# Performance work log

Measured on AMD Instinct MI355X. Metric: run time of the kernel, lower is better.

The kernel has to match this reference:

```python
import jax, jax.numpy as jnp
import numpy as np

N, C, H, K = 65432, 64, 4, 256
D = C // H
POS_BND = 20            # int((4*256)**(1/3) * 2)
RPE_NUM = 2 * POS_BND + 1


def setup_inputs() -> dict:
    key = jax.random.key(0)
    ks = jax.random.split(key, 8)
    feat = jax.random.normal(ks[0], (N, C), jnp.float32)
    qkv_w = jax.random.normal(ks[1], (3 * C, C), jnp.float32) * (C ** -0.5)
    qkv_b = jnp.zeros((3 * C,), jnp.float32)
    proj_w = jax.random.normal(ks[2], (C, C), jnp.float32) * (C ** -0.5)
    proj_b = jnp.zeros((C,), jnp.float32)
    rpe_table = jax.random.normal(ks[3], (3 * RPE_NUM, H), jnp.float32) * 0.02
    order = jax.random.permutation(ks[4], N).astype(jnp.int32)
    inverse = jnp.argsort(order).astype(jnp.int32)
    grid_coord = jax.random.randint(ks[5], (N, 3), 0, 64, jnp.int32)
    batch = jnp.sort(jax.random.randint(ks[6], (N,), 0, 4, jnp.int32))
    return {
        "feat": feat, "qkv_w": qkv_w, "qkv_b": qkv_b,
        "proj_w": proj_w, "proj_b": proj_b, "rpe_table": rpe_table,
        "order": order, "inverse": inverse,
        "grid_coord": grid_coord, "batch": batch, "num_batches": 4,
    }


def reference(feat, qkv_w, qkv_b, proj_w, proj_b, rpe_table,
              order, inverse, grid_coord, batch, num_batches):
    scale = D ** -0.5
    pad = K - N % K                      # torch pads K - N%K rows
    Npad = N + pad
    P = Npad // K                        # number of serialized patches

    # gather by serialization order, pad, window
    f = jnp.concatenate([feat[order], jnp.zeros((pad, C), feat.dtype)], 0)
    f = f.reshape(P, K, C)

    # attn mask from batch ids (pad rows get id = num_batches -> masked)
    b = jnp.concatenate([batch, jnp.full((pad,), num_batches, batch.dtype)], 0)
    b = b.reshape(P, K)
    mask = jnp.where(b[:, :, None] != b[:, None, :], -1000.0, 0.0)  # [P,K,K]

    # relative positions within each window
    gc = jnp.concatenate([grid_coord[order],
                          jnp.zeros((pad, 3), grid_coord.dtype)], 0)
    gc = gc.reshape(P, K, 3)
    rel = gc[:, :, None, :] - gc[:, None, :, :]          # [P,K,K,3]
    idx = jnp.clip(rel, -POS_BND, POS_BND) + POS_BND     # [P,K,K,3]

    # RPE bias: sum of 3 per-axis table lookups (avoids [P,K,K,3,H] blowup)
    bias = rpe_table[idx[..., 0]]
    bias = bias + rpe_table[idx[..., 1] + RPE_NUM]
    bias = bias + rpe_table[idx[..., 2] + 2 * RPE_NUM]   # [P,K,K,H]
    bias = bias.transpose(0, 3, 1, 2)                    # [P,H,K,K]

    # qkv projection and head split
    qkv = (f @ qkv_w.T + qkv_b).reshape(P, K, 3, H, D)
    qkv = qkv.transpose(2, 0, 3, 1, 4)                   # [3,P,H,K,D]
    q, k, v = qkv[0], qkv[1], qkv[2]

    attn = jnp.einsum('phid,phjd->phij', q * scale, k)
    attn = attn + bias + mask[:, None]
    attn = jax.nn.softmax(attn, axis=-1)

    out = jnp.einsum('phij,phjd->phid', attn, v)         # [P,H,K,D]
    out = out.transpose(0, 2, 1, 3).reshape(Npad, C)
    out = out[inverse][:N]                               # unserialize
    return out @ proj_w.T + proj_b
```

## Files before the change

kernel.cpp:

```cpp
#include <hip/hip_runtime.h>
#include <hip/hip_bf16.h>

#define N_PTS   65432
#define C_DIM   64
#define H_HEADS 4
#define D_HEAD  16
#define K_WIN   256
#define NPAD    65536
#define P_PATCH 256
#define POS_BND 20
#define RPE_NUM 41
#define QKV_DIM 192

__global__ __launch_bounds__(256) void qkv_kernel(
    const float* __restrict__ feat, const float* __restrict__ qkv_w,
    const float* __restrict__ qkv_b, const int* __restrict__ order,
    float* __restrict__ qkv)
{
    __shared__ float fS[64 * 68];
    __shared__ float wS[192 * 68];
    __shared__ float bS[192];

    const int t  = threadIdx.x;
    const int bx = blockIdx.x;

    #pragma unroll
    for (int s = 0; s < 48; ++s) {
        int idx = t + 256 * s;
        int row = idx >> 6, col = idx & 63;
        wS[row * 68 + col] = qkv_w[idx];
    }
    if (t < QKV_DIM) bS[t] = qkv_b[t];

    {
        int rr = t >> 2, part = t & 3;
        int r = bx * 64 + rr;
        int orig = (r < N_PTS) ? order[r] : -1;
        float4 v0, v1, v2, v3;
        if (orig >= 0) {
            const float4* fp = (const float4*)(feat + (size_t)orig * 64 + part * 16);
            v0 = fp[0]; v1 = fp[1]; v2 = fp[2]; v3 = fp[3];
        } else {
            v0 = make_float4(0.f, 0.f, 0.f, 0.f); v1 = v0; v2 = v0; v3 = v0;
        }
        float* dst = fS + rr * 68 + part * 16;
        *(float4*)(dst + 0) = v0; *(float4*)(dst + 4)  = v1;
        *(float4*)(dst + 8) = v2; *(float4*)(dst + 12) = v3;
    }
    __syncthreads();

    const int rg = t >> 4, cg = t & 15;
    float acc[4][12];
    #pragma unroll
    for (int i = 0; i < 4; ++i)
        #pragma unroll
        for (int j = 0; j < 12; ++j) acc[i][j] = 0.f;

    #pragma unroll
    for (int kk = 0; kk < 16; ++kk) {
        float4 f4[4];
        #pragma unroll
        for (int i = 0; i < 4; ++i)
            f4[i] = *(const float4*)&fS[(rg * 4 + i) * 68 + kk * 4];
        #pragma unroll
        for (int j = 0; j < 12; ++j) {
            float4 w4 = *(const float4*)&wS[(cg + 16 * j) * 68 + kk * 4];
            #pragma unroll
            for (int i = 0; i < 4; ++i) {
                acc[i][j] = fmaf(f4[i].x, w4.x, acc[i][j]);
                acc[i][j] = fmaf(f4[i].y, w4.y, acc[i][j]);
                acc[i][j] = fmaf(f4[i].z, w4.z, acc[i][j]);
                acc[i][j] = fmaf(f4[i].w, w4.w, acc[i][j]);
            }
        }
    }
    #pragma unroll
    for (int i = 0; i < 4; ++i) {
        int r = bx * 64 + rg * 4 + i;
        #pragma unroll
        for (int j = 0; j < 12; ++j) {
            int c = cg + 16 * j;
            qkv[(size_t)r * QKV_DIM + c] = acc[i][j] + bS[c];
        }
    }
}

__global__ __launch_bounds__(128) void attn_kernel(
    const float* __restrict__ qkv, const float* __restrict__ rpe_table,
    const int* __restrict__ order, const int* __restrict__ grid_coord,
    const int* __restrict__ batch, float* __restrict__ attn_out)
{
    __shared__ float kS[256 * 16];
    __shared__ float vS[256 * 16];
    __shared__ int4  gS[256];
    __shared__ float rpeS[3 * RPE_NUM];

    const int t = threadIdx.x;
    const int p = blockIdx.x, h = blockIdx.y;

    for (int rr = t; rr < 256; rr += 128) {
        int r = p * 256 + rr;
        const float* row = qkv + (size_t)r * QKV_DIM;
        #pragma unroll
        for (int d4 = 0; d4 < 4; ++d4) {
            *(float4*)&kS[rr * 16 + d4 * 4] = *(const float4*)(row + 64  + h * 16 + d4 * 4);
            *(float4*)&vS[rr * 16 + d4 * 4] = *(const float4*)(row + 128 + h * 16 + d4 * 4);
        }
        if (r < N_PTS) {
            int orig = order[r];
            gS[rr] = make_int4(grid_coord[orig * 3 + 0], grid_coord[orig * 3 + 1],
                               grid_coord[orig * 3 + 2], batch[r]);
        } else {
            gS[rr] = make_int4(0, 0, 0, -1);
        }
    }
    for (int i = t; i < 3 * RPE_NUM; i += 128) rpeS[i] = rpe_table[i * H_HEADS + h];
    __syncthreads();

    const float scale = 0.25f;
    const int r0 = p * 256 + t, r1 = r0 + 128;
    const bool ok0 = r0 < N_PTS, ok1 = r1 < N_PTS;

    float q0[16], q1[16];
    {
        const float* a = qkv + (size_t)r0 * QKV_DIM + h * 16;
        const float* b = qkv + (size_t)r1 * QKV_DIM + h * 16;
        #pragma unroll
        for (int d4 = 0; d4 < 4; ++d4) {
            float4 qa = *(const float4*)(a + d4 * 4);
            float4 qb = *(const float4*)(b + d4 * 4);
            q0[d4*4+0] = qa.x * scale; q0[d4*4+1] = qa.y * scale;
            q0[d4*4+2] = qa.z * scale; q0[d4*4+3] = qa.w * scale;
            q1[d4*4+0] = qb.x * scale; q1[d4*4+1] = qb.y * scale;
            q1[d4*4+2] = qb.z * scale; q1[d4*4+3] = qb.w * scale;
        }
    }
    const int4 g0 = gS[t], g1 = gS[t + 128];

    float m0 = -1e30f, l0 = 0.f, m1 = -1e30f, l1 = 0.f;
    float acc0[16], acc1[16];
    #pragma unroll
    for (int d = 0; d < 16; ++d) { acc0[d] = 0.f; acc1[d] = 0.f; }

    for (int j = 0; j < 256; ++j) {
        const int4 gj = gS[j];

        int dx0 = min(max(g0.x - gj.x, -POS_BND), POS_BND);
        int dy0 = min(max(g0.y - gj.y, -POS_BND), POS_BND);
        int dz0 = min(max(g0.z - gj.z, -POS_BND), POS_BND);
        float s0 = rpeS[dx0 + POS_BND] + rpeS[dy0 + POS_BND + RPE_NUM]
                 + rpeS[dz0 + POS_BND + 2 * RPE_NUM];
        s0 += (g0.w == gj.w) ? 0.f : -1000.f;

        int dx1 = min(max(g1.x - gj.x, -POS_BND), POS_BND);
        int dy1 = min(max(g1.y - gj.y, -POS_BND), POS_BND);
        int dz1 = min(max(g1.z - gj.z, -POS_BND), POS_BND);
        float s1 = rpeS[dx1 + POS_BND] + rpeS[dy1 + POS_BND + RPE_NUM]
                 + rpeS[dz1 + POS_BND + 2 * RPE_NUM];
        s1 += (g1.w == gj.w) ? 0.f : -1000.f;

        const float4* kp = (const float4*)&kS[j * 16];
        float4 k0 = kp[0], k1v = kp[1], k2 = kp[2], k3 = kp[3];
        s0 = fmaf(q0[0],  k0.x,  s0); s0 = fmaf(q0[1],  k0.y,  s0);
        s0 = fmaf(q0[2],  k0.z,  s0); s0 = fmaf(q0[3],  k0.w,  s0);
        s0 = fmaf(q0[4],  k1v.x, s0); s0 = fmaf(q0[5],  k1v.y, s0);
        s0 = fmaf(q0[6],  k1v.z, s0); s0 = fmaf(q0[7],  k1v.w, s0);
        s0 = fmaf(q0[8],  k2.x,  s0); s0 = fmaf(q0[9],  k2.y,  s0);
        s0 = fmaf(q0[10], k2.z,  s0); s0 = fmaf(q0[11], k2.w,  s0);
        s0 = fmaf(q0[12], k3.x,  s0); s0 = fmaf(q0[13], k3.y,  s0);
        s0 = fmaf(q0[14], k3.z,  s0); s0 = fmaf(q0[15], k3.w,  s0);
        s1 = fmaf(q1[0],  k0.x,  s1); s1 = fmaf(q1[1],  k0.y,  s1);
        s1 = fmaf(q1[2],  k0.z,  s1); s1 = fmaf(q1[3],  k0.w,  s1);
        s1 = fmaf(q1[4],  k1v.x, s1); s1 = fmaf(q1[5],  k1v.y, s1);
        s1 = fmaf(q1[6],  k1v.z, s1); s1 = fmaf(q1[7],  k1v.w, s1);
        s1 = fmaf(q1[8],  k2.x,  s1); s1 = fmaf(q1[9],  k2.y,  s1);
        s1 = fmaf(q1[10], k2.z,  s1); s1 = fmaf(q1[11], k2.w,  s1);
        s1 = fmaf(q1[12], k3.x,  s1); s1 = fmaf(q1[13], k3.y,  s1);
        s1 = fmaf(q1[14], k3.z,  s1); s1 = fmaf(q1[15], k3.w,  s1);

        bool nd = (s0 > m0) || (s1 > m1);
        if (__any(nd)) {
            float mn0 = fmaxf(m0, s0);
            float c0  = __expf(m0 - mn0);
            l0 *= c0;
            #pragma unroll
            for (int d = 0; d < 16; ++d) acc0[d] *= c0;
            m0 = mn0;
            float mn1 = fmaxf(m1, s1);
            float c1  = __expf(m1 - mn1);
            l1 *= c1;
            #pragma unroll
            for (int d = 0; d < 16; ++d) acc1[d] *= c1;
            m1 = mn1;
        }
        float p0 = __expf(s0 - m0); l0 += p0;
        float p1 = __expf(s1 - m1); l1 += p1;

        const float4* vp = (const float4*)&vS[j * 16];
        float4 va = vp[0], vb = vp[1], vc = vp[2], vd = vp[3];
        acc0[0]  = fmaf(p0, va.x, acc0[0]);  acc0[1]  = fmaf(p0, va.y, acc0[1]);
        acc0[2]  = fmaf(p0, va.z, acc0[2]);  acc0[3]  = fmaf(p0, va.w, acc0[3]);
        acc0[4]  = fmaf(p0, vb.x, acc0[4]);  acc0[5]  = fmaf(p0, vb.y, acc0[5]);
        acc0[6]  = fmaf(p0, vb.z, acc0[6]);  acc0[7]  = fmaf(p0, vb.w, acc0[7]);
        acc0[8]  = fmaf(p0, vc.x, acc0[8]);  acc0[9]  = fmaf(p0, vc.y, acc0[9]);
        acc0[10] = fmaf(p0, vc.z, acc0[10]); acc0[11] = fmaf(p0, vc.w, acc0[11]);
        acc0[12] = fmaf(p0, vd.x, acc0[12]); acc0[13] = fmaf(p0, vd.y, acc0[13]);
        acc0[14] = fmaf(p0, vd.z, acc0[14]); acc0[15] = fmaf(p0, vd.w, acc0[15]);
        acc1[0]  = fmaf(p1, va.x, acc1[0]);  acc1[1]  = fmaf(p1, va.y, acc1[1]);
        acc1[2]  = fmaf(p1, va.z, acc1[2]);  acc1[3]  = fmaf(p1, va.w, acc1[3]);
        acc1[4]  = fmaf(p1, vb.x, acc1[4]);  acc1[5]  = fmaf(p1, vb.y, acc1[5]);
        acc1[6]  = fmaf(p1, vb.z, acc1[6]);  acc1[7]  = fmaf(p1, vb.w, acc1[7]);
        acc1[8]  = fmaf(p1, vc.x, acc1[8]);  acc1[9]  = fmaf(p1, vc.y, acc1[9]);
        acc1[10] = fmaf(p1, vc.z, acc1[10]); acc1[11] = fmaf(p1, vc.w, acc1[11]);
        acc1[12] = fmaf(p1, vd.x, acc1[12]); acc1[13] = fmaf(p1, vd.y, acc1[13]);
        acc1[14] = fmaf(p1, vd.z, acc1[14]); acc1[15] = fmaf(p1, vd.w, acc1[15]);
    }

    if (ok0) {
        float inv = 1.0f / l0;
        float* o = attn_out + (size_t)r0 * C_DIM + h * 16;
        #pragma unroll
        for (int d = 0; d < 16; ++d) o[d] = acc0[d] * inv;
    }
    if (ok1) {
        float inv = 1.0f / l1;
        float* o = attn_out + (size_t)r1 * C_DIM + h * 16;
        #pragma unroll
        for (int d = 0; d < 16; ++d) o[d] = acc1[d] * inv;
    }
}

__global__ __launch_bounds__(256) void proj_kernel(
    const float* __restrict__ attn_out, const float* __restrict__ proj_w,
    const float* __restrict__ proj_b, const int* __restrict__ inverse,
    float* __restrict__ out)
{
    __shared__ float xS[64 * 68];
    __shared__ float wS[64 * 68];
    __shared__ float bS[64];

    const int t = threadIdx.x, bx = blockIdx.x;

    #pragma unroll
    for (int s = 0; s < 16; ++s) {
        int idx = t + 256 * s;
        int row = idx >> 6, col = idx & 63;
        wS[row * 68 + col] = proj_w[idx];
    }
    if (t < 64) bS[t] = proj_b[t];

    {
        int rr = t >> 2, part = t & 3;
        int n = bx * 64 + rr;
        int src = (n < N_PTS) ? inverse[n] : -1;
        float4 v0, v1, v2, v3;
        if (src >= 0) {
            const float4* fp = (const float4*)(attn_out + (size_t)src * 64 + part * 16);
            v0 = fp[0]; v1 = fp[1]; v2 = fp[2]; v3 = fp[3];
        } else {
            v0 = make_float4(0.f, 0.f, 0.f, 0.f); v1 = v0; v2 = v0; v3 = v0;
        }
        float* dst = xS + rr * 68 + part * 16;
        *(float4*)(dst + 0) = v0; *(float4*)(dst + 4)  = v1;
        *(float4*)(dst + 8) = v2; *(float4*)(dst + 12) = v3;
    }
    __syncthreads();

    const int rg = t >> 4, cg = t & 15;
    float acc[4][4];
    #pragma unroll
    for (int i = 0; i < 4; ++i)
        #pragma unroll
        for (int j = 0; j < 4; ++j) acc[i][j] = 0.f;

    #pragma unroll
    for (int kk = 0; kk < 16; ++kk) {
        float4 f4[4];
        #pragma unroll
        for (int i = 0; i < 4; ++i)
            f4[i] = *(const float4*)&xS[(rg * 4 + i) * 68 + kk * 4];
        #pragma unroll
        for (int j = 0; j < 4; ++j) {
            float4 w4 = *(const float4*)&wS[(cg + 16 * j) * 68 + kk * 4];
            #pragma unroll
            for (int i = 0; i < 4; ++i) {
                acc[i][j] = fmaf(f4[i].x, w4.x, acc[i][j]);
                acc[i][j] = fmaf(f4[i].y, w4.y, acc[i][j]);
                acc[i][j] = fmaf(f4[i].z, w4.z, acc[i][j]);
                acc[i][j] = fmaf(f4[i].w, w4.w, acc[i][j]);
            }
        }
    }
    #pragma unroll
    for (int i = 0; i < 4; ++i) {
        int n = bx * 64 + rg * 4 + i;
        if (n < N_PTS) {
            #pragma unroll
            for (int j = 0; j < 4; ++j) {
                int c = cg + 16 * j;
                out[(size_t)n * C_DIM + c] = acc[i][j] + bS[c];
            }
        }
    }
}

extern "C" void kernel_launch(void* const* d_in, const int* in_sizes, int n_in,
                              void* d_out, int out_size, void* d_ws, size_t ws_size,
                              hipStream_t stream)
{
    const float* feat       = (const float*)d_in[0];
    const float* qkv_w      = (const float*)d_in[1];
    const float* qkv_b      = (const float*)d_in[2];
    const float* proj_w     = (const float*)d_in[3];
    const float* proj_b     = (const float*)d_in[4];
    const float* rpe_table  = (const float*)d_in[5];
    const int*   order      = (const int*)d_in[6];
    const int*   inverse    = (const int*)d_in[7];
    const int*   grid_coord = (const int*)d_in[8];
    const int*   batch      = (const int*)d_in[9];
    float*       out        = (float*)d_out;

    float* qkv      = (float*)d_ws;
    float* attn_out = qkv + (size_t)NPAD * QKV_DIM;

    qkv_kernel<<<NPAD / 64, 256, 0, stream>>>(feat, qkv_w, qkv_b, order, qkv);
    attn_kernel<<<dim3(P_PATCH, H_HEADS), 128, 0, stream>>>(
        qkv, rpe_table, order, grid_coord, batch, attn_out);
    proj_kernel<<<(N_PTS + 63) / 64, 256, 0, stream>>>(
        attn_out, proj_w, proj_b, inverse, out);
}
```

Measured before the change: 263.0 us.

## Rewrite attention inner loop with fp16 packed dot products and tiled softmax

```diff
diff --git a/kernel.cpp b/kernel.cpp
--- a/kernel.cpp
+++ b/kernel.cpp
@@ -4,13 +4,38 @@
 #define N_PTS   65432
 #define C_DIM   64
 #define H_HEADS 4
-#define D_HEAD  16
-#define K_WIN   256
 #define NPAD    65536
 #define P_PATCH 256
 #define POS_BND 20
 #define RPE_NUM 41
 #define QKV_DIM 192
+#define LOG2E   1.44269504088896f
+
+typedef __fp16 half2_t __attribute__((ext_vector_type(2)));
+
+static __device__ __forceinline__ half2_t mk_h2(float a, float b) {
+#if __has_builtin(__builtin_amdgcn_cvt_pkrtz)
+    return __builtin_amdgcn_cvt_pkrtz(a, b);
+#else
+    half2_t r; r[0] = (__fp16)a; r[1] = (__fp16)b; return r;
+#endif
+}
+static __device__ __forceinline__ float fdot2(half2_t a, half2_t b, float c) {
+#if __has_builtin(__builtin_amdgcn_fdot2)
+    return __builtin_amdgcn_fdot2(a, b, c, false);
+#else
+    return fmaf((float)a[0], (float)b[0], fmaf((float)a[1], (float)b[1], c));
+#endif
+}
+static __device__ __forceinline__ float exp2_fast(float x) {
+#if __has_builtin(__builtin_amdgcn_exp2f)
+    return __builtin_amdgcn_exp2f(x);
+#else
+    return exp2f(x);
+#endif
+}
+
+union U4 { uint4 u; half2_t h[4]; };
 
 __global__ __launch_bounds__(256) void qkv_kernel(
     const float* __restrict__ feat, const float* __restrict__ qkv_w,
@@ -18,8 +43,8 @@
     float* __restrict__ qkv)
 {
     __shared__ float fS[64 * 68];
-    __shared__ float wS[192 * 68];
-    __shared__ float bS[192];
+    __shared__ float wS[QKV_DIM * 68];
+    __shared__ float bS[QKV_DIM];
 
     const int t  = threadIdx.x;
     const int bx = blockIdx.x;
@@ -85,148 +110,149 @@
     }
 }
 
-__global__ __launch_bounds__(128) void attn_kernel(
+__global__ __launch_bounds__(256, 4) void attn_kernel(
     const float* __restrict__ qkv, const float* __restrict__ rpe_table,
     const int* __restrict__ order, const int* __restrict__ grid_coord,
     const int* __restrict__ batch, float* __restrict__ attn_out)
 {
-    __shared__ float kS[256 * 16];
-    __shared__ float vS[256 * 16];
+    __shared__ __align__(16) uint  kS[256 * 8];
+    __shared__ __align__(16) uint  vT[128 * 16];
+    __shared__ float lutS[RPE_NUM * RPE_NUM];
+    __shared__ float zS[RPE_NUM];
     __shared__ int4  gS[256];
-    __shared__ float rpeS[3 * RPE_NUM];
 
     const int t = threadIdx.x;
     const int p = blockIdx.x, h = blockIdx.y;
-
-    for (int rr = t; rr < 256; rr += 128) {
-        int r = p * 256 + rr;
-        const float* row = qkv + (size_t)r * QKV_DIM;
-        #pragma unroll
-        for (int d4 = 0; d4 < 4; ++d4) {
-            *(float4*)&kS[rr * 16 + d4 * 4] = *(const float4*)(row + 64  + h * 16 + d4 * 4);
-            *(float4*)&vS[rr * 16 + d4 * 4] = *(const float4*)(row + 128 + h * 16 + d4 * 4);
-        }
-        if (r < N_PTS) {
-            int orig = order[r];
-            gS[rr] = make_int4(grid_coord[orig * 3 + 0], grid_coord[orig * 3 + 1],
-                               grid_coord[orig * 3 + 2], batch[r]);
-        } else {
-            gS[rr] = make_int4(0, 0, 0, -1);
-        }
-    }
-    for (int i = t; i < 3 * RPE_NUM; i += 128) rpeS[i] = rpe_table[i * H_HEADS + h];
+    const int r = p * 256 + t;
+
+    {
+        const float* kp = qkv + (size_t)r * QKV_DIM + 64 + h * 16;
+        float4 a = *(const float4*)(kp + 0), b = *(const float4*)(kp + 4);
+        float4 c = *(const float4*)(kp + 8), d = *(const float4*)(kp + 12);
+        U4 A, B;
+        A.h[0] = mk_h2(a.x, a.y); A.h[1] = mk_h2(a.z, a.w);
+        A.h[2] = mk_h2(b.x, b.y); A.h[3] = mk_h2(b.z, b.w);
+        B.h[0] = mk_h2(c.x, c.y); B.h[1] = mk_h2(c.z, c.w);
+        B.h[2] = mk_h2(d.x, d.y); B.h[3] = mk_h2(d.z, d.w);
+        *(uint4*)&kS[t * 8]     = A.u;
+        *(uint4*)&kS[t * 8 + 4] = B.u;
+    }
+    {
+        int jp = t >> 1, hf = t & 1;
+        const float* v0 = qkv + (size_t)(p * 256 + 2 * jp)     * QKV_DIM + 128 + h * 16 + hf * 8;
+        const float* v1 = qkv + (size_t)(p * 256 + 2 * jp + 1) * QKV_DIM + 128 + h * 16 + hf * 8;
+        float4 a0 = *(const float4*)(v0), b0 = *(const float4*)(v0 + 4);
+        float4 a1 = *(const float4*)(v1), b1 = *(const float4*)(v1 + 4);
+        U4 A, B;
+        A.h[0] = mk_h2(a0.x, a1.x); A.h[1] = mk_h2(a0.y, a1.y);
+        A.h[2] = mk_h2(a0.z, a1.z); A.h[3] = mk_h2(a0.w, a1.w);
+        B.h[0] = mk_h2(b0.x, b1.x); B.h[1] = mk_h2(b0.y, b1.y);
+        B.h[2] = mk_h2(b0.z, b1.z); B.h[3] = mk_h2(b0.w, b1.w);
+        *(uint4*)&vT[jp * 16 + hf * 8]     = A.u;
+        *(uint4*)&vT[jp * 16 + hf * 8 + 4] = B.u;
+    }
+    if (r < N_PTS) {
+        int orig = order[r];
+        gS[t] = make_int4(grid_coord[orig * 3 + 0], grid_coord[orig * 3 + 1],
+                          grid_coord[orig * 3 + 2], batch[r]);
+    } else {
+        gS[t] = make_int4(0, 0, 0, -1);
+    }
+    for (int i = t; i < RPE_NUM * RPE_NUM; i += 256) {
+        int a = i / RPE_NUM, b = i - a * RPE_NUM;
+        lutS[i] = (rpe_table[a * H_HEADS + h] +
+                   rpe_table[(RPE_NUM + b) * H_HEADS + h]) * LOG2E;
+    }
+    if (t < RPE_NUM) zS[t] = rpe_table[(2 * RPE_NUM + t) * H_HEADS + h] * LOG2E;
     __syncthreads();
 
-    const float scale = 0.25f;
-    const int r0 = p * 256 + t, r1 = r0 + 128;
-    const bool ok0 = r0 < N_PTS, ok1 = r1 < N_PTS;
-
-    float q0[16], q1[16];
-    {
-        const float* a = qkv + (size_t)r0 * QKV_DIM + h * 16;
-        const float* b = qkv + (size_t)r1 * QKV_DIM + h * 16;
-        #pragma unroll
-        for (int d4 = 0; d4 < 4; ++d4) {
-            float4 qa = *(const float4*)(a + d4 * 4);
-            float4 qb = *(const float4*)(b + d4 * 4);
-            q0[d4*4+0] = qa.x * scale; q0[d4*4+1] = qa.y * scale;
-            q0[d4*4+2] = qa.z * scale; q0[d4*4+3] = qa.w * scale;
-            q1[d4*4+0] = qb.x * scale; q1[d4*4+1] = qb.y * scale;
-            q1[d4*4+2] = qb.z * scale; q1[d4*4+3] = qb.w * scale;
-        }
-    }
-    const int4 g0 = gS[t], g1 = gS[t + 128];
-
-    float m0 = -1e30f, l0 = 0.f, m1 = -1e30f, l1 = 0.f;
-    float acc0[16], acc1[16];
-    #pragma unroll
-    for (int d = 0; d < 16; ++d) { acc0[d] = 0.f; acc1[d] = 0.f; }
-
-    for (int j = 0; j < 256; ++j) {
-        const int4 gj = gS[j];
-
-        int dx0 = min(max(g0.x - gj.x, -POS_BND), POS_BND);
-        int dy0 = min(max(g0.y - gj.y, -POS_BND), POS_BND);
-        int dz0 = min(max(g0.z - gj.z, -POS_BND), POS_BND);
-        float s0 = rpeS[dx0 + POS_BND] + rpeS[dy0 + POS_BND + RPE_NUM]
-                 + rpeS[dz0 + POS_BND + 2 * RPE_NUM];
-        s0 += (g0.w == gj.w) ? 0.f : -1000.f;
-
-        int dx1 = min(max(g1.x - gj.x, -POS_BND), POS_BND);
-        int dy1 = min(max(g1.y - gj.y, -POS_BND), POS_BND);
-        int dz1 = min(max(g1.z - gj.z, -POS_BND), POS_BND);
-        float s1 = rpeS[dx1 + POS_BND] + rpeS[dy1 + POS_BND + RPE_NUM]
-                 + rpeS[dz1 + POS_BND + 2 * RPE_NUM];
-        s1 += (g1.w == gj.w) ? 0.f : -1000.f;
-
-        const float4* kp = (const float4*)&kS[j * 16];
-        float4 k0 = kp[0], k1v = kp[1], k2 = kp[2], k3 = kp[3];
-        s0 = fmaf(q0[0],  k0.x,  s0); s0 = fmaf(q0[1],  k0.y,  s0);
-        s0 = fmaf(q0[2],  k0.z,  s0); s0 = fmaf(q0[3],  k0.w,  s0);
-        s0 = fmaf(q0[4],  k1v.x, s0); s0 = fmaf(q0[5],  k1v.y, s0);
-        s0 = fmaf(q0[6],  k1v.z, s0); s0 = fmaf(q0[7],  k1v.w, s0);
-        s0 = fmaf(q0[8],  k2.x,  s0); s0 = fmaf(q0[9],  k2.y,  s0);
-        s0 = fmaf(q0[10], k2.z,  s0); s0 = fmaf(q0[11], k2.w,  s0);
-        s0 = fmaf(q0[12], k3.x,  s0); s0 = fmaf(q0[13], k3.y,  s0);
-        s0 = fmaf(q0[14], k3.z,  s0); s0 = fmaf(q0[15], k3.w,  s0);
-        s1 = fmaf(q1[0],  k0.x,  s1); s1 = fmaf(q1[1],  k0.y,  s1);
-        s1 = fmaf(q1[2],  k0.z,  s1); s1 = fmaf(q1[3],  k0.w,  s1);
-        s1 = fmaf(q1[4],  k1v.x, s1); s1 = fmaf(q1[5],  k1v.y, s1);
-        s1 = fmaf(q1[6],  k1v.z, s1); s1 = fmaf(q1[7],  k1v.w, s1);
-        s1 = fmaf(q1[8],  k2.x,  s1); s1 = fmaf(q1[9],  k2.y,  s1);
-        s1 = fmaf(q1[10], k2.z,  s1); s1 = fmaf(q1[11], k2.w,  s1);
-        s1 = fmaf(q1[12], k3.x,  s1); s1 = fmaf(q1[13], k3.y,  s1);
-        s1 = fmaf(q1[14], k3.z,  s1); s1 = fmaf(q1[15], k3.w,  s1);
-
-        bool nd = (s0 > m0) || (s1 > m1);
-        if (__any(nd)) {
-            float mn0 = fmaxf(m0, s0);
-            float c0  = __expf(m0 - mn0);
-            l0 *= c0;
-            #pragma unroll
-            for (int d = 0; d < 16; ++d) acc0[d] *= c0;
-            m0 = mn0;
-            float mn1 = fmaxf(m1, s1);
-            float c1  = __expf(m1 - mn1);
-            l1 *= c1;
-            #pragma unroll
-            for (int d = 0; d < 16; ++d) acc1[d] *= c1;
-            m1 = mn1;
-        }
-        float p0 = __expf(s0 - m0); l0 += p0;
-        float p1 = __expf(s1 - m1); l1 += p1;
-
-        const float4* vp = (const float4*)&vS[j * 16];
-        float4 va = vp[0], vb = vp[1], vc = vp[2], vd = vp[3];
-        acc0[0]  = fmaf(p0, va.x, acc0[0]);  acc0[1]  = fmaf(p0, va.y, acc0[1]);
-        acc0[2]  = fmaf(p0, va.z, acc0[2]);  acc0[3]  = fmaf(p0, va.w, acc0[3]);
-        acc0[4]  = fmaf(p0, vb.x, acc0[4]);  acc0[5]  = fmaf(p0, vb.y, acc0[5]);
-        acc0[6]  = fmaf(p0, vb.z, acc0[6]);  acc0[7]  = fmaf(p0, vb.w, acc0[7]);
-        acc0[8]  = fmaf(p0, vc.x, acc0[8]);  acc0[9]  = fmaf(p0, vc.y, acc0[9]);
-        acc0[10] = fmaf(p0, vc.z, acc0[10]); acc0[11] = fmaf(p0, vc.w, acc0[11]);
-        acc0[12] = fmaf(p0, vd.x, acc0[12]); acc0[13] = fmaf(p0, vd.y, acc0[13]);
-        acc0[14] = fmaf(p0, vd.z, acc0[14]); acc0[15] = fmaf(p0, vd.w, acc0[15]);
-        acc1[0]  = fmaf(p1, va.x, acc1[0]);  acc1[1]  = fmaf(p1, va.y, acc1[1]);
-        acc1[2]  = fmaf(p1, va.z, acc1[2]);  acc1[3]  = fmaf(p1, va.w, acc1[3]);
-        acc1[4]  = fmaf(p1, vb.x, acc1[4]);  acc1[5]  = fmaf(p1, vb.y, acc1[5]);
-        acc1[6]  = fmaf(p1, vb.z, acc1[6]);  acc1[7]  = fmaf(p1, vb.w, acc1[7]);
-        acc1[8]  = fmaf(p1, vc.x, acc1[8]);  acc1[9]  = fmaf(p1, vc.y, acc1[9]);
-        acc1[10] = fmaf(p1, vc.z, acc1[10]); acc1[11] = fmaf(p1, vc.w, acc1[11]);
-        acc1[12] = fmaf(p1, vd.x, acc1[12]); acc1[13] = fmaf(p1, vd.y, acc1[13]);
-        acc1[14] = fmaf(p1, vd.z, acc1[14]); acc1[15] = fmaf(p1, vd.w, acc1[15]);
-    }
-
-    if (ok0) {
-        float inv = 1.0f / l0;
-        float* o = attn_out + (size_t)r0 * C_DIM + h * 16;
-        #pragma unroll
-        for (int d = 0; d < 16; ++d) o[d] = acc0[d] * inv;
-    }
-    if (ok1) {
-        float inv = 1.0f / l1;
-        float* o = attn_out + (size_t)r1 * C_DIM + h * 16;
-        #pragma unroll
-        for (int d = 0; d < 16; ++d) o[d] = acc1[d] * inv;
+    half2_t qh[8];
+    {
+        const float QS = 0.25f * LOG2E;
+        const float* qp = qkv + (size_t)r * QKV_DIM + h * 16;
+        float4 a = *(const float4*)(qp + 0), b = *(const float4*)(qp + 4);
+        float4 c = *(const float4*)(qp + 8), d = *(const float4*)(qp + 12);
+        qh[0] = mk_h2(a.x * QS, a.y * QS); qh[1] = mk_h2(a.z * QS, a.w * QS);
+        qh[2] = mk_h2(b.x * QS, b.y * QS); qh[3] = mk_h2(b.z * QS, b.w * QS);
+        qh[4] = mk_h2(c.x * QS, c.y * QS); qh[5] = mk_h2(c.z * QS, c.w * QS);
+        qh[6] = mk_h2(d.x * QS, d.y * QS); qh[7] = mk_h2(d.z * QS, d.w * QS);
+    }
+    const int4 gi = gS[t];
+
+    float m = -1e30f, l = 0.f;
+    float acc[16];
+    #pragma unroll
+    for (int d2 = 0; d2 < 16; ++d2) acc[d2] = 0.f;
+
+    for (int tile = 0; tile < 16; ++tile) {
+        float s[16];
+        float tmax = -1e30f;
+        #pragma unroll
+        for (int jj = 0; jj < 16; ++jj) {
+            const int j = tile * 16 + jj;
+            const int4 gj = gS[j];
+            int dx = min(max(gi.x - gj.x, -POS_BND), POS_BND) + POS_BND;
+            int dy = min(max(gi.y - gj.y, -POS_BND), POS_BND) + POS_BND;
+            int dz = min(max(gi.z - gj.z, -POS_BND), POS_BND) + POS_BND;
+            float sv = lutS[dx * RPE_NUM + dy] + zS[dz];
+            sv += (gi.w == gj.w) ? 0.f : (-1000.f * LOG2E);
+            U4 A, B;
+            A.u = *(const uint4*)&kS[j * 8];
+            B.u = *(const uint4*)&kS[j * 8 + 4];
+            sv = fdot2(A.h[0], qh[0], sv); sv = fdot2(A.h[1], qh[1], sv);
+            sv = fdot2(A.h[2], qh[2], sv); sv = fdot2(A.h[3], qh[3], sv);
+            sv = fdot2(B.h[0], qh[4], sv); sv = fdot2(B.h[1], qh[5], sv);
+            sv = fdot2(B.h[2], qh[6], sv); sv = fdot2(B.h[3], qh[7], sv);
+            s[jj] = sv;
+            tmax = fmaxf(tmax, sv);
+        }
+        float mn = fmaxf(m, tmax);
+        float cr = exp2_fast(m - mn);
+        l *= cr;
+        #pragma unroll
+        for (int d2 = 0; d2 < 16; ++d2) acc[d2] *= cr;
+        m = mn;
+
+        half2_t pp[8];
+        #pragma unroll
+        for (int u = 0; u < 8; ++u) {
+            float p0 = exp2_fast(s[2 * u]     - m);
+            float p1 = exp2_fast(s[2 * u + 1] - m);
+            l += p0 + p1;
+            pp[u] = mk_h2(p0, p1);
+        }
+        #pragma unroll
+        for (int u = 0; u < 8; ++u) {
+            const int jp = tile * 8 + u;
+            U4 A, B, C, D;
+            A.u = *(const uint4*)&vT[jp * 16 + 0];
+            B.u = *(const uint4*)&vT[jp * 16 + 4];
+            C.u = *(const uint4*)&vT[jp * 16 + 8];
+            D.u = *(const uint4*)&vT[jp * 16 + 12];
+            acc[0]  = fdot2(pp[u], A.h[0], acc[0]);
+            acc[1]  = fdot2(pp[u], A.h[1], acc[1]);
+            acc[2]  = fdot2(pp[u], A.h[2], acc[2]);
+            acc[3]  = fdot2(pp[u], A.h[3], acc[3]);
+            acc[4]  = fdot2(pp[u], B.h[0], acc[4]);
+            acc[5]  = fdot2(pp[u], B.h[1], acc[5]);
+            acc[6]  = fdot2(pp[u], B.h[2], acc[6]);
+            acc[7]  = fdot2(pp[u], B.h[3], acc[7]);
+            acc[8]  = fdot2(pp[u], C.h[0], acc[8]);
+            acc[9]  = fdot2(pp[u], C.h[1], acc[9]);
+            acc[10] = fdot2(pp[u], C.h[2], acc[10]);
+            acc[11] = fdot2(pp[u], C.h[3], acc[11]);
+            acc[12] = fdot2(pp[u], D.h[0], acc[12]);
+            acc[13] = fdot2(pp[u], D.h[1], acc[13]);
+            acc[14] = fdot2(pp[u], D.h[2], acc[14]);
+            acc[15] = fdot2(pp[u], D.h[3], acc[15]);
+        }
+    }
+
+    if (r < N_PTS) {
+        float inv = 1.0f / l;
+        float* o = attn_out + (size_t)r * C_DIM + h * 16;
+        #pragma unroll
+        for (int d2 = 0; d2 < 16; ++d2) o[d2] = acc[d2] * inv;
     }
 }
 
@@ -324,7 +350,7 @@
     float* attn_out = qkv + (size_t)NPAD * QKV_DIM;
 
     qkv_kernel<<<NPAD / 64, 256, 0, stream>>>(feat, qkv_w, qkv_b, order, qkv);
-    attn_kernel<<<dim3(P_PATCH, H_HEADS), 128, 0, stream>>>(
+    attn_kernel<<<dim3(P_PATCH, H_HEADS), 256, 0, stream>>>(
         qkv, rpe_table, order, grid_coord, batch, attn_out);
     proj_kernel<<<(N_PTS + 63) / 64, 256, 0, stream>>>(
         attn_out, proj_w, proj_b, inverse, out);
```

Result: faster. 223.2 us (-15.1%).
